# Kernel tuning notes

Measured on AMD Instinct MI355X. Metric: run time of the kernel, lower is better.

Reference implementation:

```python
import jax, jax.numpy as jnp
import numpy as np

N_NODES = 16384
N_EDGES = 65536
B = 256
L = 1000
BN_EPS = 1e-5


def _bn_last(h, g, b, m, v):
    # BatchNorm1d in eval mode over last (feature) axis
    return (h - m) / jnp.sqrt(v + BN_EPS) * g + b


def _bn_chan(h, g, b, m, v):
    # BatchNorm1d in eval mode over channel axis of [N, C, W]
    inv = g / jnp.sqrt(v + BN_EPS)
    return (h - m[None, :, None]) * inv[None, :, None] + b[None, :, None]


def _conv1d(x, W, b):
    # x: [N, C, W], W: [O, I, K], stride 1, VALID
    y = jax.lax.conv_general_dilated(x, W, (1,), 'VALID',
                                     dimension_numbers=('NCH', 'OIH', 'NCH'))
    return y + b[None, :, None]


def _forward(x, g1_W1, g1_b1, g1_W2, g1_b2, gW1, gb1, gW2, gb2,
             bn_gamma, bn_beta, bn_mean, bn_var, fcxd_W, fcxd_b, embed,
             c1_W, c1_b, c2_W, c2_b, c3_W, c3_b,
             cbn_gamma, cbn_beta, cbn_mean, cbn_var, fcxc_W, fcxc_b,
             bnfc_gamma, bnfc_beta, bnfc_mean, bnfc_var,
             fc1_W, fc1_b, fc2_W, fc2_b, out_W, out_b,
             edge_index, batch, target):
    src, dst = edge_index[0], edge_index[1]
    # GIN layer 1: out_i = MLP(x_i + sum_{j->i} x_j)  (eps = 0)
    agg = jax.ops.segment_sum(x[src], dst, num_segments=N_NODES)
    h = x + agg
    h = jnp.maximum(h @ g1_W1 + g1_b1, 0.0) @ g1_W2 + g1_b2
    h = _bn_last(jnp.maximum(h, 0.0), bn_gamma[0], bn_beta[0], bn_mean[0], bn_var[0])
    # GIN layers 2..5 (stacked params)
    for i in range(4):
        agg = jax.ops.segment_sum(h[src], dst, num_segments=N_NODES)
        t = h + agg
        t = jnp.maximum(t @ gW1[i] + gb1[i], 0.0) @ gW2[i] + gb2[i]
        h = _bn_last(jnp.maximum(t, 0.0), bn_gamma[i + 1], bn_beta[i + 1],
                     bn_mean[i + 1], bn_var[i + 1])
    # global_add_pool over graph ids
    pooled = jax.ops.segment_sum(h, batch, num_segments=B)          # [B, 32]
    xd = jnp.maximum(pooled @ fcxd_W + fcxd_b, 0.0)                 # [B, 128] (dropout: eval)
    # protein branch
    emb = embed[target]                                             # [B, L, 128]
    xd2 = jnp.broadcast_to(xd[:, None, :], (B, L, xd.shape[-1]))
    xc = jnp.concatenate([emb, xd2], axis=-1).transpose(0, 2, 1)    # [B, 256, L]
    conv_params = [(c1_W, c1_b), (c2_W, c2_b), (c3_W, c3_b)]
    for i in range(3):
        xc = _conv1d(xc, conv_params[i][0], conv_params[i][1])
        xc = jnp.maximum(_bn_chan(xc, cbn_gamma[i], cbn_beta[i],
                                  cbn_mean[i], cbn_var[i]), 0.0)
    xcm = jnp.max(xc, axis=-1)                                      # global max pool -> [B, 32]
    xcf = jnp.maximum(_bn_last(xcm @ fcxc_W + fcxc_b,
                               bnfc_gamma, bnfc_beta, bnfc_mean, bnfc_var), 0.0)
    z = jnp.concatenate([xd, xcf], axis=1)                          # [B, 256]
    z = jnp.maximum(z @ fc1_W + fc1_b, 0.0)
    z = jnp.maximum(z @ fc2_W + fc2_b, 0.0)
    return z @ out_W + out_b                                        # [B, 1]


def setup_inputs() -> dict:
    key = jax.random.key(0)
    ks = list(jax.random.split(key, 48))
    it = iter(range(48))
    f32 = jnp.float32

    def rn(sh, s=0.1):
        return jax.random.normal(ks[next(it)], sh, dtype=f32) * s

    def un(sh):
        return jax.random.uniform(ks[next(it)], sh, dtype=f32, minval=0.5, maxval=1.5)

    inp = {}
    inp['x'] = jax.random.normal(ks[next(it)], (N_NODES, 78), dtype=f32)
    inp['edge_index'] = jax.random.randint(ks[next(it)], (2, N_EDGES), 0, N_NODES, dtype=jnp.int32)
    inp['batch'] = jnp.sort(jax.random.randint(ks[next(it)], (N_NODES,), 0, B, dtype=jnp.int32))
    inp['target'] = jax.random.randint(ks[next(it)], (B, L), 0, 26, dtype=jnp.int32)
    inp['g1_W1'] = rn((78, 32)); inp['g1_b1'] = rn((32,))
    inp['g1_W2'] = rn((32, 32)); inp['g1_b2'] = rn((32,))
    inp['gW1'] = rn((4, 32, 32)); inp['gb1'] = rn((4, 32))
    inp['gW2'] = rn((4, 32, 32)); inp['gb2'] = rn((4, 32))
    inp['bn_gamma'] = un((5, 32)); inp['bn_beta'] = rn((5, 32))
    inp['bn_mean'] = rn((5, 32)); inp['bn_var'] = un((5, 32))
    inp['fcxd_W'] = rn((32, 128)); inp['fcxd_b'] = rn((128,))
    inp['embed'] = rn((26, 128), 1.0)
    inp['c1_W'] = rn((32, 256, 16)); inp['c1_b'] = rn((32,))
    inp['c2_W'] = rn((32, 32, 16)); inp['c2_b'] = rn((32,))
    inp['c3_W'] = rn((32, 32, 16)); inp['c3_b'] = rn((32,))
    inp['cbn_gamma'] = un((3, 32)); inp['cbn_beta'] = rn((3, 32))
    inp['cbn_mean'] = rn((3, 32)); inp['cbn_var'] = un((3, 32))
    inp['fcxc_W'] = rn((32, 128)); inp['fcxc_b'] = rn((128,))
    inp['bnfc_gamma'] = un((128,)); inp['bnfc_beta'] = rn((128,))
    inp['bnfc_mean'] = rn((128,)); inp['bnfc_var'] = un((128,))
    inp['fc1_W'] = rn((256, 1024)); inp['fc1_b'] = rn((1024,))
    inp['fc2_W'] = rn((1024, 256)); inp['fc2_b'] = rn((256,))
    inp['out_W'] = rn((256, 1)); inp['out_b'] = rn((1,))
    return inp


def reference(x, edge_index, batch, target, g1_W1, g1_b1, g1_W2, g1_b2,
              gW1, gb1, gW2, gb2, bn_gamma, bn_beta, bn_mean, bn_var,
              fcxd_W, fcxd_b, embed, c1_W, c1_b, c2_W, c2_b, c3_W, c3_b,
              cbn_gamma, cbn_beta, cbn_mean, cbn_var, fcxc_W, fcxc_b,
              bnfc_gamma, bnfc_beta, bnfc_mean, bnfc_var,
              fc1_W, fc1_b, fc2_W, fc2_b, out_W, out_b):
    return _forward(x, g1_W1, g1_b1, g1_W2, g1_b2, gW1, gb1, gW2, gb2,
                    bn_gamma, bn_beta, bn_mean, bn_var, fcxd_W, fcxd_b, embed,
                    c1_W, c1_b, c2_W, c2_b, c3_W, c3_b,
                    cbn_gamma, cbn_beta, cbn_mean, cbn_var, fcxc_W, fcxc_b,
                    bnfc_gamma, bnfc_beta, bnfc_mean, bnfc_var,
                    fc1_W, fc1_b, fc2_W, fc2_b, out_W, out_b,
                    edge_index, batch, target)
```

## Files before the change

### kernel.cpp

```cpp
#include <hip/hip_runtime.h>
#include <hip/hip_bf16.h>

typedef __hip_bfloat16 bf16;
__device__ __forceinline__ float b2f(bf16 v){ return __bfloat162float(v); }

typedef __attribute__((ext_vector_type(8))) short s8v;
typedef __attribute__((ext_vector_type(4))) float f4v;

#define N_NODES 16384
#define N_EDGES 65536
#define NB 256
#define LSEQ 1000
#define BN_EPS 1e-5f
#define W1O 985
#define W2O 970
#define W3O 955

__device__ int g_isf32;

__device__ __forceinline__ float LD(const void* p, int i, int f){
    return f ? ((const float*)p)[i] : b2f(((const bf16*)p)[i]);
}

__device__ __forceinline__ unsigned short f2b(float x){
    unsigned u = __float_as_uint(x);
    return (unsigned short)((u + 0x7FFFu + ((u >> 16) & 1u)) >> 16);
}
__device__ __forceinline__ float bb2f(unsigned short h){
    return __uint_as_float(((unsigned)h) << 16);
}

__device__ float g_hA[N_NODES*32];
__device__ float g_hB[N_NODES*32];
__device__ float g_xd[NB*128];
__device__ float g_P[16*26*32];
__device__ float g_wsum[32*128];
__device__ float g_xdb[NB*32];
__device__ float g_xcm[NB*32];
__device__ __attribute__((aligned(16))) unsigned short g_wf[2][32768];
__device__ int g_deg[N_NODES];
__device__ int g_cur[N_NODES];
__device__ int g_rowptr[N_NODES + 1];
__device__ int g_csrc[N_EDGES];
__device__ int g_gstart[NB + 1];

#define PREP_BLOCKS 2305

__global__ __launch_bounds__(256) void k_prep(
    const void* x, const int* __restrict__ ei, const int* __restrict__ batch,
    const void* g1W1)
{
    __shared__ float sW1[78*32];
    __shared__ float sx[8][78];
    __shared__ int s_cnt;
    int tid = threadIdx.x, bid = blockIdx.x;

    if (tid == 0) s_cnt = 0;
    __syncthreads();
    {
        const unsigned short* u = (const unsigned short*)x;
        int bad = 0;
        for (int i = tid; i < 512; i += 256){
            unsigned short h = u[i];
            int ex = (h >> 7) & 0xFF;
            if (!(h == 0 || (ex >= 96 && ex <= 142))) bad++;
        }
        if (bad) atomicAdd(&s_cnt, bad);
    }
    __syncthreads();
    const int F = (s_cnt > 50) ? 1 : 0;
    if (bid == 0 && tid == 0) g_isf32 = F;

    if (bid < 1){
        int b = tid;
        int lo = 0, hi = N_NODES;
        while (lo < hi){ int mid = (lo + hi) >> 1; if (batch[mid] < b) lo = mid + 1; else hi = mid; }
        g_gstart[b] = lo;
        if (b == 0) g_gstart[NB] = N_NODES;
    } else if (bid < 257){
        int e = (bid - 1)*256 + tid;
        atomicAdd(&g_deg[ei[N_EDGES + e]], 1);
    } else {
        for (int i = tid; i < 78*32; i += 256) sW1[i] = LD(g1W1, i, F);
        int nodeBase = (bid - 257)*8;
        for (int i = tid; i < 8*78; i += 256){
            int ln = i / 78, f = i - ln*78;
            sx[ln][f] = LD(x, (nodeBase + ln)*78 + f, F);
        }
        __syncthreads();
        int ln = tid >> 5, j = tid & 31;
        float a = 0.f;
        #pragma unroll 6
        for (int i = 0; i < 78; i++) a += sx[ln][i] * sW1[i*32 + j];
        g_hA[(nodeBase + ln)*32 + j] = a;
    }
}

__global__ __launch_bounds__(1024) void k_scan(){
    __shared__ int part[1024];
    int t = threadIdx.x;
    int base = t*16;
    int s = 0;
    #pragma unroll
    for (int i = 0; i < 16; i++) s += g_deg[base + i];
    part[t] = s;
    __syncthreads();
    for (int off = 1; off < 1024; off <<= 1){
        int v = (t >= off) ? part[t - off] : 0;
        __syncthreads();
        part[t] += v;
        __syncthreads();
    }
    int run = (t == 0) ? 0 : part[t - 1];
    for (int i = 0; i < 16; i++){
        g_rowptr[base + i] = run;
        g_cur[base + i] = run;
        run += g_deg[base + i];
        g_deg[base + i] = 0;
    }
    if (t == 1023) g_rowptr[N_NODES] = run;
}
__global__ void k_fill(const int* __restrict__ ei){
    int e = blockIdx.x*256 + threadIdx.x;
    int d = ei[N_EDGES + e];
    int slot = atomicAdd(&g_cur[d], 1);
    g_csrc[slot] = ei[e];
}

__device__ __forceinline__ float csr_gather(const float* hin, int n, int j){
    int rs = g_rowptr[n];
    int deg = g_rowptr[n + 1] - rs;
    float agg = 0.f;
    for (int base = 0; base < deg; base += 32){
        int cnt = deg - base; if (cnt > 32) cnt = 32;
        int myidx = (j < cnt) ? g_csrc[rs + base + j] : 0;
        for (int e = 0; e < cnt; e++){
            int src = __shfl(myidx, e, 32);
            agg += hin[src*32 + j];
        }
    }
    return agg;
}

#define GIN1B_GIN 2048
#define GIN1B_EXTRA 356

__global__ __launch_bounds__(256) void k_gin1b(
    const void* b1, const void* W2, const void* b2,
    const void* bng, const void* bnb, const void* bnm, const void* bnv,
    const void* embed, const void* c1W, const void* c2W, const void* c3W)
{
    const int F = g_isf32;
    int tid = threadIdx.x, bid = blockIdx.x;

    if (bid >= GIN1B_GIN){
        int t = bid - GIN1B_GIN;
        if (t < 256){
            int idx = t*256 + tid;
            int sel = idx >> 15;
            int r = idx & 32767;
            int j = r & 7;
            int lane = (r >> 3) & 63;
            int hl = (r >> 9) & 1;
            int ogrp = (r >> 10) & 1;
            int ktg = r >> 11;
            int c = (lane >> 4)*8 + j;
            int o = ogrp*16 + (lane & 15);
            const void* Wt = sel ? c3W : c2W;
            float wv = LD(Wt, o*512 + c*16 + ktg, F);
            unsigned short h = f2b(wv);
            g_wf[sel][r] = hl ? f2b(wv - bb2f(h)) : h;
        } else if (t < 308){
            int idx = (t - 256)*256 + tid;
            int k = idx & 15, o = (idx >> 4) & 31, tt = idx >> 9;
            float acc = 0.f;
            for (int c = 0; c < 128; c++)
                acc += LD(embed, tt*128 + c, F) * LD(c1W, o*4096 + c*16 + k, F);
            g_P[(k*26 + tt)*32 + o] = acc;
        } else if (t < 324){
            int idx = (t - 308)*256 + tid;
            int o = idx >> 7, c = idx & 127;
            float a = 0.f;
            #pragma unroll
            for (int k = 0; k < 16; k++) a += LD(c1W, o*4096 + (128 + c)*16 + k, F);
            g_wsum[o*128 + c] = a;
        } else {
            int i = (t - 324)*256 + tid;
            g_xcm[i] = 0.f;
        }
        return;
    }

    __shared__ float sW2[32*32];
    __shared__ float sb1[32], sb2[32], sA[32], sB[32];
    __shared__ float st[8][32];
    for (int i = tid; i < 1024; i += 256) sW2[i] = LD(W2, i, F);
    if (tid < 32){
        sb1[tid] = LD(b1, tid, F); sb2[tid] = LD(b2, tid, F);
        float inv = LD(bng, tid, F) * rsqrtf(LD(bnv, tid, F) + BN_EPS);
        sA[tid] = inv;
        sB[tid] = LD(bnb, tid, F) - LD(bnm, tid, F) * inv;
    }
    __syncthreads();
    int ln = tid >> 5, j = tid & 31;
    int n = bid*8 + ln;
    float agg = csr_gather(g_hA, n, j);
    st[ln][j] = fmaxf(g_hA[n*32 + j] + agg + sb1[j], 0.f);
    __syncthreads();
    float t2 = sb2[j];
    #pragma unroll
    for (int i = 0; i < 32; i++) t2 += st[ln][i] * sW2[i*32 + j];
    t2 = fmaxf(t2, 0.f);
    g_hB[n*32 + j] = t2 * sA[j] + sB[j];
}

__global__ __launch_bounds__(256) void k_gin32L(
    const void* W1, const void* b1, const void* W2, const void* b2,
    const void* bng, const void* bnb, const void* bnm, const void* bnv, int l)
{
    const int F = g_isf32;
    const float* hin = (l & 1) ? g_hA : g_hB;
    float* hout = (l & 1) ? g_hB : g_hA;
    const int oW = l*1024, ob = l*32, obn = (l+1)*32;
    __shared__ float sW1[32*32], sW2[32*32];
    __shared__ float sb1[32], sb2[32], sA[32], sB[32];
    __shared__ float sh[8][32], st[8][32];
    int tid = threadIdx.x;
    for (int i = tid; i < 1024; i += 256){ sW1[i] = LD(W1, oW + i, F); sW2[i] = LD(W2, oW + i, F); }
    if (tid < 32){
        sb1[tid] = LD(b1, ob + tid, F); sb2[tid] = LD(b2, ob + tid, F);
        float inv = LD(bng, obn + tid, F) * rsqrtf(LD(bnv, obn + tid, F) + BN_EPS);
        sA[tid] = inv;
        sB[tid] = LD(bnb, obn + tid, F) - LD(bnm, obn + tid, F) * inv;
    }
    int ln = tid >> 5, j = tid & 31;
    int n = blockIdx.x*8 + ln;
    float agg = csr_gather(hin, n, j);
    sh[ln][j] = hin[n*32 + j] + agg;
    __syncthreads();
    float t1 = sb1[j];
    #pragma unroll
    for (int i = 0; i < 32; i++) t1 += sh[ln][i] * sW1[i*32 + j];
    st[ln][j] = fmaxf(t1, 0.f);
    __syncthreads();
    float t2 = sb2[j];
    #pragma unroll
    for (int i = 0; i < 32; i++) t2 += st[ln][i] * sW2[i*32 + j];
    t2 = fmaxf(t2, 0.f);
    hout[n*32 + j] = t2 * sA[j] + sB[j];
}

__global__ __launch_bounds__(256) void k_poolxd(const void* W, const void* bias,
                                                const void* c1b){
    const int F = g_isf32;
    __shared__ float red[8][32];
    __shared__ float sxd[128];
    int b = blockIdx.x, tid = threadIdx.x;
    int j = tid & 31, sub = tid >> 5;
    int s = g_gstart[b], e = g_gstart[b + 1];
    float a = 0.f;
    for (int n = s + sub; n < e; n += 8) a += g_hB[n*32 + j];
    red[sub][j] = a;
    __syncthreads();
    if (sub == 0){
        red[0][j] = red[0][j] + red[1][j] + red[2][j] + red[3][j]
                  + red[4][j] + red[5][j] + red[6][j] + red[7][j];
    }
    __syncthreads();
    if (tid < 128){
        float acc = LD(bias, tid, F);
        #pragma unroll
        for (int i = 0; i < 32; i++) acc += red[0][i] * LD(W, i*128 + tid, F);
        float xdv = fmaxf(acc, 0.f);
        g_xd[b*128 + tid] = xdv;
        sxd[tid] = xdv;
    }
    __syncthreads();
    if (tid < 32){
        float a2 = LD(c1b, tid, F);
        for (int c = 0; c < 128; c++) a2 += sxd[c] * g_wsum[tid*128 + c];
        g_xdb[b*32 + tid] = a2;
    }
}


#define FT_W 128
#define C1R 160
#define C2R 144
#define CPAD 40
#define STGN 176

__global__ __launch_bounds__(512, 6) void k_cfuse(
    const int* __restrict__ target,
    const void* g, const void* be, const void* m, const void* v,
    const void* c2b, const void* c3b)
{
    const int F = g_isf32;
    __shared__ int stg[STGN];
    __shared__ __attribute__((aligned(16))) unsigned short sC1h[C1R*CPAD];
    __shared__ __attribute__((aligned(16))) unsigned short sC1l[C1R*CPAD];
    __shared__ __attribute__((aligned(16))) unsigned short sC2h[C2R*CPAD];
    __shared__ __attribute__((aligned(16))) unsigned short sC2l[C2R*CPAD];
    __shared__ float sxb[32], sA1[32], sB1[32], sSc2[32], sOf2[32], sSc3[32], sOf3[32];
    int b = blockIdx.x >> 3;
    int tile = blockIdx.x & 7;
    int wbase = tile * FT_W;
    int tid = threadIdx.x;

    for (int i = tid; i < STGN; i += 512){
        int gi = wbase + i;
        stg[i] = (gi < LSEQ) ? target[b*LSEQ + gi] : 0;
    }
    if (tid < 32){
        sxb[tid] = g_xdb[b*32 + tid];
        float i1 = LD(g, tid, F) * rsqrtf(LD(v, tid, F) + BN_EPS);
        sA1[tid] = i1;
        sB1[tid] = LD(be, tid, F) - LD(m, tid, F) * i1;
        float i2 = LD(g, 32 + tid, F) * rsqrtf(LD(v, 32 + tid, F) + BN_EPS);
        sSc2[tid] = i2;
        sOf2[tid] = LD(be, 32 + tid, F) + (LD(c2b, tid, F) - LD(m, 32 + tid, F)) * i2;
        float i3 = LD(g, 64 + tid, F) * rsqrtf(LD(v, 64 + tid, F) + BN_EPS);
        sSc3[tid] = i3;
        sOf3[tid] = LD(be, 64 + tid, F) + (LD(c3b, tid, F) - LD(m, 64 + tid, F)) * i3;
    }
    __syncthreads();

    {
        int o = tid & 31, rsub = tid >> 5;
        float iA = sA1[o], iB = sB1[o], xb = sxb[o];
        for (int r0 = rsub; r0 < C1R; r0 += 32){
            int r1 = r0 + 16;
            float a0 = xb, a1 = xb;
            #pragma unroll
            for (int k = 0; k < 16; k++){
                a0 += g_P[(k*26 + stg[r0 + k])*32 + o];
                a1 += g_P[(k*26 + stg[r1 + k])*32 + o];
            }
            float v0 = (wbase + r0 < W1O) ? fmaxf(a0 * iA + iB, 0.f) : 0.f;
            float v1 = (wbase + r1 < W1O) ? fmaxf(a1 * iA + iB, 0.f) : 0.f;
            unsigned short h0 = f2b(v0), h1 = f2b(v1);
            sC1h[r0*CPAD + o] = h0;
            sC1l[r0*CPAD + o] = f2b(v0 - bb2f(h0));
            sC1h[r1*CPAD + o] = h1;
            sC1l[r1*CPAD + o] = f2b(v1 - bb2f(h1));
        }
    }
    __syncthreads();

    int lane = tid & 63;
    int wv = tid >> 6;
    int ml = lane & 15, quad = lane >> 4;
    int ogrp = wv & 1;
    int part = wv >> 1;
    int oo = ogrp*16 + ml;

    {
        const s8v* wfb = (const s8v*)&g_wf[0][0] + ogrp*128 + lane;
        int nmt = (part == 0) ? 3 : 2;
        f4v acc[3];
        #pragma unroll
        for (int i = 0; i < 3; i++) acc[i] = (f4v){0.f,0.f,0.f,0.f};
        s8v bhA = wfb[0],   blA = wfb[64];
        s8v bhB = wfb[256], blB = wfb[320];
        for (int ktg = 0; ktg < 16; ktg += 2){
            s8v ch = bhA, cl = blA;
            if (ktg + 2 < 16){ bhA = wfb[(ktg+2)*256]; blA = wfb[(ktg+2)*256 + 64]; }
            #pragma unroll
            for (int i = 0; i < 3; i++){
                if (i < nmt){
                    int row = (part + 4*i)*16 + ml + ktg;
                    int aidx = row*CPAD + quad*8;
                    s8v ah = *(const s8v*)&sC1h[aidx];
                    s8v al = *(const s8v*)&sC1l[aidx];
                    acc[i] = __builtin_amdgcn_mfma_f32_16x16x32_bf16(ah, ch, acc[i], 0, 0, 0);
                    acc[i] = __builtin_amdgcn_mfma_f32_16x16x32_bf16(ah, cl, acc[i], 0, 0, 0);
                    acc[i] = __builtin_amdgcn_mfma_f32_16x16x32_bf16(al, ch, acc[i], 0, 0, 0);
                }
            }
            s8v dh = bhB, dl = blB;
            if (ktg + 3 < 16){ bhB = wfb[(ktg+3)*256]; blB = wfb[(ktg+3)*256 + 64]; }
            #pragma unroll
            for (int i = 0; i < 3; i++){
                if (i < nmt){
                    int row = (part + 4*i)*16 + ml + ktg + 1;
                    int aidx = row*CPAD + quad*8;
                    s8v ah = *(const s8v*)&sC1h[aidx];
                    s8v al = *(const s8v*)&sC1l[aidx];
                    acc[i] = __builtin_amdgcn_mfma_f32_16x16x32_bf16(ah, dh, acc[i], 0, 0, 0);
                    acc[i] = __builtin_amdgcn_mfma_f32_16x16x32_bf16(ah, dl, acc[i], 0, 0, 0);
                    acc[i] = __builtin_amdgcn_mfma_f32_16x16x32_bf16(al, dh, acc[i], 0, 0, 0);
                }
            }
        }
        float sc = sSc2[oo], of = sOf2[oo];
        #pragma unroll
        for (int i = 0; i < 3; i++){
            if (i < nmt){
                int mt = part + 4*i;
                f4v a = acc[i];
                float ys[4] = {a.x, a.y, a.z, a.w};
                #pragma unroll
                for (int rr = 0; rr < 4; rr++){
                    int row = mt*16 + quad*4 + rr;
                    float y = fmaxf(ys[rr]*sc + of, 0.f);
                    unsigned short h = f2b(y);
                    sC2h[row*CPAD + oo] = h;
                    sC2l[row*CPAD + oo] = f2b(y - bb2f(h));
                }
            }
        }
    }
    __syncthreads();

    {
        const s8v* wfb = (const s8v*)&g_wf[1][0] + ogrp*128 + lane;
        f4v acc[2];
        #pragma unroll
        for (int i = 0; i < 2; i++) acc[i] = (f4v){0.f,0.f,0.f,0.f};
        s8v bhA = wfb[0],   blA = wfb[64];
        s8v bhB = wfb[256], blB = wfb[320];
        for (int ktg = 0; ktg < 16; ktg += 2){
            s8v ch = bhA, cl = blA;
            if (ktg + 2 < 16){ bhA = wfb[(ktg+2)*256]; blA = wfb[(ktg+2)*256 + 64]; }
            #pragma unroll
            for (int i = 0; i < 2; i++){
                int row = (part + 4*i)*16 + ml + ktg;
                int aidx = row*CPAD + quad*8;
                s8v ah = *(const s8v*)&sC2h[aidx];
                s8v al = *(const s8v*)&sC2l[aidx];
                acc[i] = __builtin_amdgcn_mfma_f32_16x16x32_bf16(ah, ch, acc[i], 0, 0, 0);
                acc[i] = __builtin_amdgcn_mfma_f32_16x16x32_bf16(ah, cl, acc[i], 0, 0, 0);
                acc[i] = __builtin_amdgcn_mfma_f32_16x16x32_bf16(al, ch, acc[i], 0, 0, 0);
            }
            s8v dh = bhB, dl = blB;
            if (ktg + 3 < 16){ bhB = wfb[(ktg+3)*256]; blB = wfb[(ktg+3)*256 + 64]; }
            #pragma unroll
            for (int i = 0; i < 2; i++){
                int row = (part + 4*i)*16 + ml + ktg + 1;
                int aidx = row*CPAD + quad*8;
                s8v ah = *(const s8v*)&sC2h[aidx];
                s8v al = *(const s8v*)&sC2l[aidx];
                acc[i] = __builtin_amdgcn_mfma_f32_16x16x32_bf16(ah, dh, acc[i], 0, 0, 0);
                acc[i] = __builtin_amdgcn_mfma_f32_16x16x32_bf16(ah, dl, acc[i], 0, 0, 0);
                acc[i] = __builtin_amdgcn_mfma_f32_16x16x32_bf16(al, dh, acc[i], 0, 0, 0);
            }
        }
        float sc = sSc3[oo], of = sOf3[oo];
        #pragma unroll
        for (int i = 0; i < 2; i++){
            int mt = part + 4*i;
            int w0 = wbase + mt*16 + quad*4;
            f4v a = acc[i];
            float y0 = fmaxf(a.x*sc + of, 0.f);
            float y1 = fmaxf(a.y*sc + of, 0.f);
            float y2 = fmaxf(a.z*sc + of, 0.f);
            float y3 = fmaxf(a.w*sc + of, 0.f);
            if (w0 < W3O){
                float mx = y0;
                if (w0+1 < W3O) mx = fmaxf(mx, y1);
                if (w0+2 < W3O) mx = fmaxf(mx, y2);
                if (w0+3 < W3O) mx = fmaxf(mx, y3);
                atomicMax((int*)&g_xcm[b*32 + oo], __float_as_int(mx));
            }
        }
    }
}


__global__ __launch_bounds__(1024) void k_tail(
    const void* fcxcW, const void* fcxcb,
    const void* bg, const void* bb, const void* bm, const void* bv,
    const void* fc1W, const void* fc1b,
    const void* fc2W, const void* fc2b,
    const void* outW, const void* outb, void* out)
{
    const int F = g_isf32;
    __shared__ float sz[256];
    __shared__ float z1s[1024];
    __shared__ float sp[4][256];
    int b = blockIdx.x, t = threadIdx.x;
    if (t < 128) sz[t] = g_xd[b*128 + t];
    else if (t < 256){
        int j = t - 128;
        float a = LD(fcxcb, j, F);
        #pragma unroll
        for (int i = 0; i < 32; i++) a += g_xcm[b*32 + i] * LD(fcxcW, i*128 + j, F);
        float inv = LD(bg, j, F) * rsqrtf(LD(bv, j, F) + BN_EPS);
        a = (a - LD(bm, j, F)) * inv + LD(bb, j, F);
        sz[t] = fmaxf(a, 0.f);
    }
    __syncthreads();
    float a = LD(fc1b, t, F);
    for (int i = 0; i < 256; i++) a += sz[i] * LD(fc1W, i*1024 + t, F);
    z1s[t] = fmaxf(a, 0.f);
    __syncthreads();
    int j = t & 255, kq = t >> 8;
    float a2 = 0.f;
    #pragma unroll 8
    for (int i = 0; i < 256; i++)
        a2 += z1s[kq*256 + i] * LD(fc2W, (kq*256 + i)*256 + j, F);
    sp[kq][j] = a2;
    __syncthreads();
    if (t < 256){
        float z2 = fmaxf(sp[0][t] + sp[1][t] + sp[2][t] + sp[3][t] + LD(fc2b, t, F), 0.f);
        sp[0][t] = z2 * LD(outW, t, F);
    }
    __syncthreads();
    for (int s = 128; s > 0; s >>= 1){
        if (t < s) sp[0][t] += sp[0][t + s];
        __syncthreads();
    }
    if (t == 0){
        float r = sp[0][0] + LD(outb, 0, F);
        if (F) ((float*)out)[b] = r;
        else   ((bf16*)out)[b] = __float2bfloat16(r);
    }
}


extern "C" void kernel_launch(void* const* d_in, const int* in_sizes, int n_in,
                              void* d_out, int out_size, void* d_ws, size_t ws_size,
                              hipStream_t stream)
{
    (void)in_sizes; (void)n_in; (void)out_size; (void)d_ws; (void)ws_size;
    const void* x      = d_in[0];
    const int*  ei     = (const int*)d_in[1];
    const int*  batch  = (const int*)d_in[2];
    const int*  target = (const int*)d_in[3];
    const void* g1W1 = d_in[4];  const void* g1b1 = d_in[5];
    const void* g1W2 = d_in[6];  const void* g1b2 = d_in[7];
    const void* gW1  = d_in[8];  const void* gb1  = d_in[9];
    const void* gW2  = d_in[10]; const void* gb2  = d_in[11];
    const void* bng  = d_in[12]; const void* bnb  = d_in[13];
    const void* bnm  = d_in[14]; const void* bnv  = d_in[15];
    const void* fcxdW = d_in[16]; const void* fcxdb = d_in[17];
    const void* embed = d_in[18];
    const void* c1W = d_in[19]; const void* c1b = d_in[20];
    const void* c2W = d_in[21]; const void* c2b = d_in[22];
    const void* c3W = d_in[23]; const void* c3b = d_in[24];
    const void* cbng = d_in[25]; const void* cbnb = d_in[26];
    const void* cbnm = d_in[27]; const void* cbnv = d_in[28];
    const void* fcxcW = d_in[29]; const void* fcxcb = d_in[30];
    const void* bnfcg = d_in[31]; const void* bnfcb = d_in[32];
    const void* bnfcm = d_in[33]; const void* bnfcv = d_in[34];
    const void* fc1W = d_in[35]; const void* fc1b = d_in[36];
    const void* fc2W = d_in[37]; const void* fc2b = d_in[38];
    const void* outW = d_in[39]; const void* outb = d_in[40];

    k_prep<<<PREP_BLOCKS, 256, 0, stream>>>(x, ei, batch, g1W1);
    k_scan<<<1, 1024, 0, stream>>>();
    k_fill<<<N_EDGES/256, 256, 0, stream>>>(ei);
    k_gin1b<<<GIN1B_GIN + GIN1B_EXTRA, 256, 0, stream>>>(
        g1b1, g1W2, g1b2, bng, bnb, bnm, bnv, embed, c1W, c2W, c3W);
    for (int l = 0; l < 4; l++){
        k_gin32L<<<N_NODES/8, 256, 0, stream>>>(gW1, gb1, gW2, gb2,
                                                bng, bnb, bnm, bnv, l);
    }
    k_poolxd<<<NB, 256, 0, stream>>>(fcxdW, fcxdb, c1b);
    k_cfuse<<<NB*8, 512, 0, stream>>>(target, cbng, cbnb, cbnm, cbnv, c2b, c3b);
    k_tail<<<NB, 1024, 0, stream>>>(fcxcW, fcxcb, bnfcg, bnfcb, bnfcm, bnfcv,
                                    fc1W, fc1b, fc2W, fc2b, outW, outb, d_out);
}
```

Baseline: 400.5 us.

## Remap conv MFMA waves to cover both output groups, batch two samples per tail block

In the fused conv kernel, each wave now computes both 16-channel output groups for its own 16-row tile. Each A fragment loaded from LDS is therefore reused across two weight fragments, which replaces the old split where waves covered 2-3 interleaved row tiles of a single output group. The aim is fewer LDS reads per MFMA and less loop-control overhead, at the cost of uneven work, since wave 0 handles an extra tile. The tail MLP kernel now processes two batch samples per block so each fc1/fc2 weight load is shared, halving weight traffic but also halving the number of blocks.

Measured after the change: 427.0 us. 1.07x slower.

```diff
diff --git a/kernel.cpp b/kernel.cpp
--- a/kernel.cpp
+++ b/kernel.cpp
@@ -290,6 +290,8 @@
 #define CPAD 40
 #define STGN 176
 
+#define MFMA_BF16 __builtin_amdgcn_mfma_f32_16x16x32_bf16
+
 __global__ __launch_bounds__(512, 6) void k_cfuse(
     const int* __restrict__ target,
     const void* g, const void* be, const void* m, const void* v,
@@ -350,118 +352,128 @@
     int lane = tid & 63;
     int wv = tid >> 6;
     int ml = lane & 15, quad = lane >> 4;
-    int ogrp = wv & 1;
-    int part = wv >> 1;
-    int oo = ogrp*16 + ml;
 
     {
-        const s8v* wfb = (const s8v*)&g_wf[0][0] + ogrp*128 + lane;
-        int nmt = (part == 0) ? 3 : 2;
-        f4v acc[3];
-        #pragma unroll
-        for (int i = 0; i < 3; i++) acc[i] = (f4v){0.f,0.f,0.f,0.f};
-        s8v bhA = wfb[0],   blA = wfb[64];
-        s8v bhB = wfb[256], blB = wfb[320];
-        for (int ktg = 0; ktg < 16; ktg += 2){
-            s8v ch = bhA, cl = blA;
-            if (ktg + 2 < 16){ bhA = wfb[(ktg+2)*256]; blA = wfb[(ktg+2)*256 + 64]; }
+        const s8v* wf0 = (const s8v*)&g_wf[0][0] + lane;
+        const s8v* wf1 = (const s8v*)&g_wf[0][0] + 128 + lane;
+        int has2 = (wv == 0);
+        f4v a00 = (f4v){0.f,0.f,0.f,0.f}, a01 = (f4v){0.f,0.f,0.f,0.f};
+        f4v a10 = (f4v){0.f,0.f,0.f,0.f}, a11 = (f4v){0.f,0.f,0.f,0.f};
+        s8v nh0 = wf0[0], nl0 = wf0[64];
+        s8v nh1 = wf1[0], nl1 = wf1[64];
+        for (int ktg = 0; ktg < 16; ktg++){
+            s8v bh0 = nh0, bl0 = nl0, bh1 = nh1, bl1 = nl1;
+            if (ktg < 15){
+                nh0 = wf0[(ktg+1)*256]; nl0 = wf0[(ktg+1)*256 + 64];
+                nh1 = wf1[(ktg+1)*256]; nl1 = wf1[(ktg+1)*256 + 64];
+            }
+            {
+                int row = wv*16 + ml + ktg;
+                int aidx = row*CPAD + quad*8;
+                s8v ah = *(const s8v*)&sC1h[aidx];
+                s8v al = *(const s8v*)&sC1l[aidx];
+                a00 = MFMA_BF16(ah, bh0, a00, 0, 0, 0);
+                a00 = MFMA_BF16(ah, bl0, a00, 0, 0, 0);
+                a00 = MFMA_BF16(al, bh0, a00, 0, 0, 0);
+                a01 = MFMA_BF16(ah, bh1, a01, 0, 0, 0);
+                a01 = MFMA_BF16(ah, bl1, a01, 0, 0, 0);
+                a01 = MFMA_BF16(al, bh1, a01, 0, 0, 0);
+            }
+            if (has2){
+                int row = 128 + ml + ktg;
+                int aidx = row*CPAD + quad*8;
+                s8v ah = *(const s8v*)&sC1h[aidx];
+                s8v al = *(const s8v*)&sC1l[aidx];
+                a10 = MFMA_BF16(ah, bh0, a10, 0, 0, 0);
+                a10 = MFMA_BF16(ah, bl0, a10, 0, 0, 0);
+                a10 = MFMA_BF16(al, bh0, a10, 0, 0, 0);
+                a11 = MFMA_BF16(ah, bh1, a11, 0, 0, 0);
+                a11 = MFMA_BF16(ah, bl1, a11, 0, 0, 0);
+                a11 = MFMA_BF16(al, bh1, a11, 0, 0, 0);
+            }
+        }
+        float sc0 = sSc2[ml],      of0 = sOf2[ml];
+        float sc1 = sSc2[16 + ml], of1 = sOf2[16 + ml];
+        {
+            float y00[4] = {a00.x, a00.y, a00.z, a00.w};
+            float y01[4] = {a01.x, a01.y, a01.z, a01.w};
             #pragma unroll
-            for (int i = 0; i < 3; i++){
-                if (i < nmt){
-                    int row = (part + 4*i)*16 + ml + ktg;
-                    int aidx = row*CPAD + quad*8;
-                    s8v ah = *(const s8v*)&sC1h[aidx];
-                    s8v al = *(const s8v*)&sC1l[aidx];
-                    acc[i] = __builtin_amdgcn_mfma_f32_16x16x32_bf16(ah, ch, acc[i], 0, 0, 0);
-                    acc[i] = __builtin_amdgcn_mfma_f32_16x16x32_bf16(ah, cl, acc[i], 0, 0, 0);
-                    acc[i] = __builtin_amdgcn_mfma_f32_16x16x32_bf16(al, ch, acc[i], 0, 0, 0);
-                }
+            for (int rr = 0; rr < 4; rr++){
+                int row = wv*16 + quad*4 + rr;
+                float u0 = fmaxf(y00[rr]*sc0 + of0, 0.f);
+                unsigned short h0 = f2b(u0);
+                sC2h[row*CPAD + ml] = h0;
+                sC2l[row*CPAD + ml] = f2b(u0 - bb2f(h0));
+                float u1 = fmaxf(y01[rr]*sc1 + of1, 0.f);
+                unsigned short h1 = f2b(u1);
+                sC2h[row*CPAD + 16 + ml] = h1;
+                sC2l[row*CPAD + 16 + ml] = f2b(u1 - bb2f(h1));
             }
-            s8v dh = bhB, dl = blB;
-            if (ktg + 3 < 16){ bhB = wfb[(ktg+3)*256]; blB = wfb[(ktg+3)*256 + 64]; }
+        }
+        if (has2){
+            float y10[4] = {a10.x, a10.y, a10.z, a10.w};
+            float y11[4] = {a11.x, a11.y, a11.z, a11.w};
             #pragma unroll
-            for (int i = 0; i < 3; i++){
-                if (i < nmt){
-                    int row = (part + 4*i)*16 + ml + ktg + 1;
-                    int aidx = row*CPAD + quad*8;
-                    s8v ah = *(const s8v*)&sC1h[aidx];
-                    s8v al = *(const s8v*)&sC1l[aidx];
-                    acc[i] = __builtin_amdgcn_mfma_f32_16x16x32_bf16(ah, dh, acc[i], 0, 0, 0);
-                    acc[i] = __builtin_amdgcn_mfma_f32_16x16x32_bf16(ah, dl, acc[i], 0, 0, 0);
-                    acc[i] = __builtin_amdgcn_mfma_f32_16x16x32_bf16(al, dh, acc[i], 0, 0, 0);
-                }
+            for (int rr = 0; rr < 4; rr++){
+                int row = 128 + quad*4 + rr;
+                float u0 = fmaxf(y10[rr]*sc0 + of0, 0.f);
+                unsigned short h0 = f2b(u0);
+                sC2h[row*CPAD + ml] = h0;
+                sC2l[row*CPAD + ml] = f2b(u0 - bb2f(h0));
+                float u1 = fmaxf(y11[rr]*sc1 + of1, 0.f);
+                unsigned short h1 = f2b(u1);
+                sC2h[row*CPAD + 16 + ml] = h1;
+                sC2l[row*CPAD + 16 + ml] = f2b(u1 - bb2f(h1));
             }
         }
-        float sc = sSc2[oo], of = sOf2[oo];
-        #pragma unroll
-        for (int i = 0; i < 3; i++){
-            if (i < nmt){
-                int mt = part + 4*i;
-                f4v a = acc[i];
-                float ys[4] = {a.x, a.y, a.z, a.w};
-                #pragma unroll
-                for (int rr = 0; rr < 4; rr++){
-                    int row = mt*16 + quad*4 + rr;
-                    float y = fmaxf(ys[rr]*sc + of, 0.f);
-                    unsigned short h = f2b(y);
-                    sC2h[row*CPAD + oo] = h;
-                    sC2l[row*CPAD + oo] = f2b(y - bb2f(h));
-                }
+    }
+    __syncthreads();
+
+    {
+        const s8v* wf0 = (const s8v*)&g_wf[1][0] + lane;
+        const s8v* wf1 = (const s8v*)&g_wf[1][0] + 128 + lane;
+        f4v c0 = (f4v){0.f,0.f,0.f,0.f}, c1 = (f4v){0.f,0.f,0.f,0.f};
+        s8v nh0 = wf0[0], nl0 = wf0[64];
+        s8v nh1 = wf1[0], nl1 = wf1[64];
+        for (int ktg = 0; ktg < 16; ktg++){
+            s8v bh0 = nh0, bl0 = nl0, bh1 = nh1, bl1 = nl1;
+            if (ktg < 15){
+                nh0 = wf0[(ktg+1)*256]; nl0 = wf0[(ktg+1)*256 + 64];
+                nh1 = wf1[(ktg+1)*256]; nl1 = wf1[(ktg+1)*256 + 64];
             }
-        }
-    }
-    __syncthreads();
-
-    {
-        const s8v* wfb = (const s8v*)&g_wf[1][0] + ogrp*128 + lane;
-        f4v acc[2];
-        #pragma unroll
-        for (int i = 0; i < 2; i++) acc[i] = (f4v){0.f,0.f,0.f,0.f};
-        s8v bhA = wfb[0],   blA = wfb[64];
-        s8v bhB = wfb[256], blB = wfb[320];
-        for (int ktg = 0; ktg < 16; ktg += 2){
-            s8v ch = bhA, cl = blA;
-            if (ktg + 2 < 16){ bhA = wfb[(ktg+2)*256]; blA = wfb[(ktg+2)*256 + 64]; }
-            #pragma unroll
-            for (int i = 0; i < 2; i++){
-                int row = (part + 4*i)*16 + ml + ktg;
-                int aidx = row*CPAD + quad*8;
-                s8v ah = *(const s8v*)&sC2h[aidx];
-                s8v al = *(const s8v*)&sC2l[aidx];
-                acc[i] = __builtin_amdgcn_mfma_f32_16x16x32_bf16(ah, ch, acc[i], 0, 0, 0);
-                acc[i] = __builtin_amdgcn_mfma_f32_16x16x32_bf16(ah, cl, acc[i], 0, 0, 0);
-                acc[i] = __builtin_amdgcn_mfma_f32_16x16x32_bf16(al, ch, acc[i], 0, 0, 0);
-            }
-            s8v dh = bhB, dl = blB;
-            if (ktg + 3 < 16){ bhB = wfb[(ktg+3)*256]; blB = wfb[(ktg+3)*256 + 64]; }
-            #pragma unroll
-            for (int i = 0; i < 2; i++){
-                int row = (part + 4*i)*16 + ml + ktg + 1;
-                int aidx = row*CPAD + quad*8;
-                s8v ah = *(const s8v*)&sC2h[aidx];
-                s8v al = *(const s8v*)&sC2l[aidx];
-                acc[i] = __builtin_amdgcn_mfma_f32_16x16x32_bf16(ah, dh, acc[i], 0, 0, 0);
-                acc[i] = __builtin_amdgcn_mfma_f32_16x16x32_bf16(ah, dl, acc[i], 0, 0, 0);
-                acc[i] = __builtin_amdgcn_mfma_f32_16x16x32_bf16(al, dh, acc[i], 0, 0, 0);
-            }
-        }
-        float sc = sSc3[oo], of = sOf3[oo];
-        #pragma unroll
-        for (int i = 0; i < 2; i++){
-            int mt = part + 4*i;
-            int w0 = wbase + mt*16 + quad*4;
-            f4v a = acc[i];
-            float y0 = fmaxf(a.x*sc + of, 0.f);
-            float y1 = fmaxf(a.y*sc + of, 0.f);
-            float y2 = fmaxf(a.z*sc + of, 0.f);
-            float y3 = fmaxf(a.w*sc + of, 0.f);
-            if (w0 < W3O){
-                float mx = y0;
-                if (w0+1 < W3O) mx = fmaxf(mx, y1);
-                if (w0+2 < W3O) mx = fmaxf(mx, y2);
-                if (w0+3 < W3O) mx = fmaxf(mx, y3);
-                atomicMax((int*)&g_xcm[b*32 + oo], __float_as_int(mx));
-            }
+            int row = wv*16 + ml + ktg;
+            int aidx = row*CPAD + quad*8;
+            s8v ah = *(const s8v*)&sC2h[aidx];
+            s8v al = *(const s8v*)&sC2l[aidx];
+            c0 = MFMA_BF16(ah, bh0, c0, 0, 0, 0);
+            c0 = MFMA_BF16(ah, bl0, c0, 0, 0, 0);
+            c0 = MFMA_BF16(al, bh0, c0, 0, 0, 0);
+            c1 = MFMA_BF16(ah, bh1, c1, 0, 0, 0);
+            c1 = MFMA_BF16(ah, bl1, c1, 0, 0, 0);
+            c1 = MFMA_BF16(al, bh1, c1, 0, 0, 0);
+        }
+        float sc0 = sSc3[ml],      of0 = sOf3[ml];
+        float sc1 = sSc3[16 + ml], of1 = sOf3[16 + ml];
+        int w0 = wbase + wv*16 + quad*4;
+        if (w0 < W3O){
+            float p0 = fmaxf(c0.x*sc0 + of0, 0.f);
+            float p1 = fmaxf(c0.y*sc0 + of0, 0.f);
+            float p2 = fmaxf(c0.z*sc0 + of0, 0.f);
+            float p3 = fmaxf(c0.w*sc0 + of0, 0.f);
+            float mx = p0;
+            if (w0+1 < W3O) mx = fmaxf(mx, p1);
+            if (w0+2 < W3O) mx = fmaxf(mx, p2);
+            if (w0+3 < W3O) mx = fmaxf(mx, p3);
+            atomicMax((int*)&g_xcm[b*32 + ml], __float_as_int(mx));
+            float q0 = fmaxf(c1.x*sc1 + of1, 0.f);
+            float q1 = fmaxf(c1.y*sc1 + of1, 0.f);
+            float q2 = fmaxf(c1.z*sc1 + of1, 0.f);
+            float q3 = fmaxf(c1.w*sc1 + of1, 0.f);
+            float my = q0;
+            if (w0+1 < W3O) my = fmaxf(my, q1);
+            if (w0+2 < W3O) my = fmaxf(my, q2);
+            if (w0+3 < W3O) my = fmaxf(my, q3);
+            atomicMax((int*)&g_xcm[b*32 + 16 + ml], __float_as_int(my));
         }
     }
 }
@@ -475,45 +487,74 @@
     const void* outW, const void* outb, void* out)
 {
     const int F = g_isf32;
-    __shared__ float sz[256];
-    __shared__ float z1s[1024];
-    __shared__ float sp[4][256];
-    int b = blockIdx.x, t = threadIdx.x;
-    if (t < 128) sz[t] = g_xd[b*128 + t];
-    else if (t < 256){
+    __shared__ float sz0[256], sz1[256];
+    __shared__ float z1s0[1024], z1s1[1024];
+    __shared__ float sp0[4][256], sp1[4][256];
+    int b0 = blockIdx.x*2, b1 = b0 + 1, t = threadIdx.x;
+    if (t < 128){
+        sz0[t] = g_xd[b0*128 + t];
+        sz1[t] = g_xd[b1*128 + t];
+    } else if (t < 256){
         int j = t - 128;
-        float a = LD(fcxcb, j, F);
+        float a0 = LD(fcxcb, j, F), a1 = a0;
         #pragma unroll
-        for (int i = 0; i < 32; i++) a += g_xcm[b*32 + i] * LD(fcxcW, i*128 + j, F);
+        for (int i = 0; i < 32; i++){
+            float w = LD(fcxcW, i*128 + j, F);
+            a0 += g_xcm[b0*32 + i] * w;
+            a1 += g_xcm[b1*32 + i] * w;
+        }
         float inv = LD(bg, j, F) * rsqrtf(LD(bv, j, F) + BN_EPS);
-        a = (a - LD(bm, j, F)) * inv + LD(bb, j, F);
-        sz[t] = fmaxf(a, 0.f);
-    }
-    __syncthreads();
-    float a = LD(fc1b, t, F);
-    for (int i = 0; i < 256; i++) a += sz[i] * LD(fc1W, i*1024 + t, F);
-    z1s[t] = fmaxf(a, 0.f);
+        float bm_ = LD(bm, j, F), bb_ = LD(bb, j, F);
+        sz0[t] = fmaxf((a0 - bm_) * inv + bb_, 0.f);
+        sz1[t] = fmaxf((a1 - bm_) * inv + bb_, 0.f);
+    }
+    __syncthreads();
+    {
+        float a0 = LD(fc1b, t, F), a1 = a0;
+        for (int i = 0; i < 256; i++){
+            float w = LD(fc1W, i*1024 + t, F);
+            a0 += sz0[i] * w;
+            a1 += sz1[i] * w;
+        }
+        z1s0[t] = fmaxf(a0, 0.f);
+        z1s1[t] = fmaxf(a1, 0.f);
+    }
     __syncthreads();
     int j = t & 255, kq = t >> 8;
-    float a2 = 0.f;
-    #pragma unroll 8
-    for (int i = 0; i < 256; i++)
-        a2 += z1s[kq*256 + i] * LD(fc2W, (kq*256 + i)*256 + j, F);
-    sp[kq][j] = a2;
+    {
+        float a20 = 0.f, a21 = 0.f;
+        #pragma unroll 8
+        for (int i = 0; i < 256; i++){
+            float w = LD(fc2W, (kq*256 + i)*256 + j, F);
+            a20 += z1s0[kq*256 + i] * w;
+            a21 += z1s1[kq*256 + i] * w;
+        }
+        sp0[kq][j] = a20;
+        sp1[kq][j] = a21;
+    }
     __syncthreads();
     if (t < 256){
-        float z2 = fmaxf(sp[0][t] + sp[1][t] + sp[2][t] + sp[3][t] + LD(fc2b, t, F), 0.f);
-        sp[0][t] = z2 * LD(outW, t, F);
+        float bias = LD(fc2b, t, F), ow = LD(outW, t, F);
+        float z20 = fmaxf(sp0[0][t] + sp0[1][t] + sp0[2][t] + sp0[3][t] + bias, 0.f);
+        float z21 = fmaxf(sp1[0][t] + sp1[1][t] + sp1[2][t] + sp1[3][t] + bias, 0.f);
+        sp0[0][t] = z20 * ow;
+        sp1[0][t] = z21 * ow;
     }
     __syncthreads();
     for (int s = 128; s > 0; s >>= 1){
-        if (t < s) sp[0][t] += sp[0][t + s];
+        if (t < s){
+            sp0[0][t] += sp0[0][t + s];
+            sp1[0][t] += sp1[0][t + s];
+        }
         __syncthreads();
     }
     if (t == 0){
-        float r = sp[0][0] + LD(outb, 0, F);
-        if (F) ((float*)out)[b] = r;
-        else   ((bf16*)out)[b] = __float2bfloat16(r);
+        float ob = LD(outb, 0, F);
+        float r0 = sp0[0][0] + ob;
+        float r1 = sp1[0][0] + ob;
+        if (F){ ((float*)out)[b0] = r0; ((float*)out)[b1] = r1; }
+        else  { ((bf16*)out)[b0] = __float2bfloat16(r0);
+                ((bf16*)out)[b1] = __float2bfloat16(r1); }
     }
 }
 
@@ -558,6 +599,6 @@
     }
     k_poolxd<<<NB, 256, 0, stream>>>(fcxdW, fcxdb, c1b);
     k_cfuse<<<NB*8, 512, 0, stream>>>(target, cbng, cbnb, cbnm, cbnv, c2b, c3b);
-    k_tail<<<NB, 1024, 0, stream>>>(fcxcW, fcxcb, bnfcg, bnfcb, bnfcm, bnfcv,
-                                    fc1W, fc1b, fc2W, fc2b, outW, outb, d_out);
-}
+    k_tail<<<NB/2, 1024, 0, stream>>>(fcxcW, fcxcb, bnfcg, bnfcb, bnfcm, bnfcv,
+                                      fc1W, fc1b, fc2W, fc2b, outW, outb, d_out);
+}
```

## Fuse pooling into conv and tail kernels; process two graphs per tail block

Applied to the files above, without the earlier changes.

Removes the separate pooling/xd kernel. Each conv tile block now recomputes the graph pooling, the xd projection and the conv1 bias contribution itself, and the tail kernel recomputes pooling and xd too. The tail kernel now handles two graphs per block so each fc1/fc2 weight load is shared by two samples. This saves one launch and halves weight traffic in the tail, at the cost of redundant pooling work (8x in the conv kernel) and more shared memory.

After: 414.4 us. 3.5% more time.

```diff
diff --git a/kernel.cpp b/kernel.cpp
--- a/kernel.cpp
+++ b/kernel.cpp
@@ -32,10 +32,8 @@
 
 __device__ float g_hA[N_NODES*32];
 __device__ float g_hB[N_NODES*32];
-__device__ float g_xd[NB*128];
 __device__ float g_P[16*26*32];
 __device__ float g_wsum[32*128];
-__device__ float g_xdb[NB*32];
 __device__ float g_xcm[NB*32];
 __device__ __attribute__((aligned(16))) unsigned short g_wf[2][32768];
 __device__ int g_deg[N_NODES];
@@ -250,39 +248,6 @@
     hout[n*32 + j] = t2 * sA[j] + sB[j];
 }
 
-__global__ __launch_bounds__(256) void k_poolxd(const void* W, const void* bias,
-                                                const void* c1b){
-    const int F = g_isf32;
-    __shared__ float red[8][32];
-    __shared__ float sxd[128];
-    int b = blockIdx.x, tid = threadIdx.x;
-    int j = tid & 31, sub = tid >> 5;
-    int s = g_gstart[b], e = g_gstart[b + 1];
-    float a = 0.f;
-    for (int n = s + sub; n < e; n += 8) a += g_hB[n*32 + j];
-    red[sub][j] = a;
-    __syncthreads();
-    if (sub == 0){
-        red[0][j] = red[0][j] + red[1][j] + red[2][j] + red[3][j]
-                  + red[4][j] + red[5][j] + red[6][j] + red[7][j];
-    }
-    __syncthreads();
-    if (tid < 128){
-        float acc = LD(bias, tid, F);
-        #pragma unroll
-        for (int i = 0; i < 32; i++) acc += red[0][i] * LD(W, i*128 + tid, F);
-        float xdv = fmaxf(acc, 0.f);
-        g_xd[b*128 + tid] = xdv;
-        sxd[tid] = xdv;
-    }
-    __syncthreads();
-    if (tid < 32){
-        float a2 = LD(c1b, tid, F);
-        for (int c = 0; c < 128; c++) a2 += sxd[c] * g_wsum[tid*128 + c];
-        g_xdb[b*32 + tid] = a2;
-    }
-}
-
 
 #define FT_W 128
 #define C1R 160
@@ -293,7 +258,8 @@
 __global__ __launch_bounds__(512, 6) void k_cfuse(
     const int* __restrict__ target,
     const void* g, const void* be, const void* m, const void* v,
-    const void* c2b, const void* c3b)
+    const void* c2b, const void* c3b,
+    const void* fcxdW, const void* fcxdb, const void* c1b)
 {
     const int F = g_isf32;
     __shared__ int stg[STGN];
@@ -302,6 +268,8 @@
     __shared__ __attribute__((aligned(16))) unsigned short sC2h[C2R*CPAD];
     __shared__ __attribute__((aligned(16))) unsigned short sC2l[C2R*CPAD];
     __shared__ float sxb[32], sA1[32], sB1[32], sSc2[32], sOf2[32], sSc3[32], sOf3[32];
+    __shared__ float pred[8][32];
+    __shared__ float pxd[128];
     int b = blockIdx.x >> 3;
     int tile = blockIdx.x & 7;
     int wbase = tile * FT_W;
@@ -312,7 +280,6 @@
         stg[i] = (gi < LSEQ) ? target[b*LSEQ + gi] : 0;
     }
     if (tid < 32){
-        sxb[tid] = g_xdb[b*32 + tid];
         float i1 = LD(g, tid, F) * rsqrtf(LD(v, tid, F) + BN_EPS);
         sA1[tid] = i1;
         sB1[tid] = LD(be, tid, F) - LD(m, tid, F) * i1;
@@ -322,6 +289,34 @@
         float i3 = LD(g, 64 + tid, F) * rsqrtf(LD(v, 64 + tid, F) + BN_EPS);
         sSc3[tid] = i3;
         sOf3[tid] = LD(be, 64 + tid, F) + (LD(c3b, tid, F) - LD(m, 64 + tid, F)) * i3;
+    }
+    {
+        int s = g_gstart[b], e = g_gstart[b + 1];
+        if (tid < 256){
+            int j = tid & 31, sub = tid >> 5;
+            float a = 0.f;
+            for (int n = s + sub; n < e; n += 8) a += g_hB[n*32 + j];
+            pred[sub][j] = a;
+        }
+        __syncthreads();
+        if (tid < 32){
+            int j = tid;
+            pred[0][j] = pred[0][j] + pred[1][j] + pred[2][j] + pred[3][j]
+                       + pred[4][j] + pred[5][j] + pred[6][j] + pred[7][j];
+        }
+        __syncthreads();
+        if (tid < 128){
+            float acc = LD(fcxdb, tid, F);
+            #pragma unroll
+            for (int i = 0; i < 32; i++) acc += pred[0][i] * LD(fcxdW, i*128 + tid, F);
+            pxd[tid] = fmaxf(acc, 0.f);
+        }
+        __syncthreads();
+        if (tid < 32){
+            float a2 = LD(c1b, tid, F);
+            for (int c = 0; c < 128; c++) a2 += pxd[c] * g_wsum[tid*128 + c];
+            sxb[tid] = a2;
+        }
     }
     __syncthreads();
 
@@ -472,48 +467,107 @@
     const void* bg, const void* bb, const void* bm, const void* bv,
     const void* fc1W, const void* fc1b,
     const void* fc2W, const void* fc2b,
-    const void* outW, const void* outb, void* out)
+    const void* outW, const void* outb, void* out,
+    const void* fcxdW, const void* fcxdb)
 {
     const int F = g_isf32;
-    __shared__ float sz[256];
-    __shared__ float z1s[1024];
-    __shared__ float sp[4][256];
-    int b = blockIdx.x, t = threadIdx.x;
-    if (t < 128) sz[t] = g_xd[b*128 + t];
-    else if (t < 256){
+    __shared__ float red0[8][32], red1[8][32];
+    __shared__ float sz0[256], sz1[256];
+    __shared__ float z1s0[1024], z1s1[1024];
+    __shared__ float sp0[4][256], sp1[4][256];
+    int b0 = blockIdx.x*2, b1 = b0 + 1, t = threadIdx.x;
+
+    if (t < 512){
+        int j = t & 31, sub = (t >> 5) & 7;
+        int bg_ = (t < 256) ? b0 : b1;
+        int s = g_gstart[bg_], e = g_gstart[bg_ + 1];
+        float a = 0.f;
+        for (int n = s + sub; n < e; n += 8) a += g_hB[n*32 + j];
+        if (t < 256) red0[sub][j] = a; else red1[sub][j] = a;
+    }
+    __syncthreads();
+    if (t < 32){
+        int j = t;
+        red0[0][j] = red0[0][j] + red0[1][j] + red0[2][j] + red0[3][j]
+                   + red0[4][j] + red0[5][j] + red0[6][j] + red0[7][j];
+    } else if (t < 64){
+        int j = t - 32;
+        red1[0][j] = red1[0][j] + red1[1][j] + red1[2][j] + red1[3][j]
+                   + red1[4][j] + red1[5][j] + red1[6][j] + red1[7][j];
+    }
+    __syncthreads();
+    if (t < 128){
+        float acc = LD(fcxdb, t, F);
+        #pragma unroll
+        for (int i = 0; i < 32; i++) acc += red0[0][i] * LD(fcxdW, i*128 + t, F);
+        sz0[t] = fmaxf(acc, 0.f);
+    } else if (t < 256){
         int j = t - 128;
-        float a = LD(fcxcb, j, F);
+        float acc = LD(fcxdb, j, F);
         #pragma unroll
-        for (int i = 0; i < 32; i++) a += g_xcm[b*32 + i] * LD(fcxcW, i*128 + j, F);
+        for (int i = 0; i < 32; i++) acc += red1[0][i] * LD(fcxdW, i*128 + j, F);
+        sz1[j] = fmaxf(acc, 0.f);
+    } else if (t < 384){
+        int j = t - 256;
+        float a0 = LD(fcxcb, j, F), a1 = a0;
+        #pragma unroll
+        for (int i = 0; i < 32; i++){
+            float w = LD(fcxcW, i*128 + j, F);
+            a0 += g_xcm[b0*32 + i] * w;
+            a1 += g_xcm[b1*32 + i] * w;
+        }
         float inv = LD(bg, j, F) * rsqrtf(LD(bv, j, F) + BN_EPS);
-        a = (a - LD(bm, j, F)) * inv + LD(bb, j, F);
-        sz[t] = fmaxf(a, 0.f);
-    }
-    __syncthreads();
-    float a = LD(fc1b, t, F);
-    for (int i = 0; i < 256; i++) a += sz[i] * LD(fc1W, i*1024 + t, F);
-    z1s[t] = fmaxf(a, 0.f);
+        float bm_ = LD(bm, j, F), bb_ = LD(bb, j, F);
+        sz0[128 + j] = fmaxf((a0 - bm_) * inv + bb_, 0.f);
+        sz1[128 + j] = fmaxf((a1 - bm_) * inv + bb_, 0.f);
+    }
+    __syncthreads();
+    {
+        float a0 = LD(fc1b, t, F), a1 = a0;
+        for (int i = 0; i < 256; i++){
+            float w = LD(fc1W, i*1024 + t, F);
+            a0 += sz0[i] * w;
+            a1 += sz1[i] * w;
+        }
+        z1s0[t] = fmaxf(a0, 0.f);
+        z1s1[t] = fmaxf(a1, 0.f);
+    }
     __syncthreads();
     int j = t & 255, kq = t >> 8;
-    float a2 = 0.f;
-    #pragma unroll 8
-    for (int i = 0; i < 256; i++)
-        a2 += z1s[kq*256 + i] * LD(fc2W, (kq*256 + i)*256 + j, F);
-    sp[kq][j] = a2;
+    {
+        float a20 = 0.f, a21 = 0.f;
+        #pragma unroll 8
+        for (int i = 0; i < 256; i++){
+            float w = LD(fc2W, (kq*256 + i)*256 + j, F);
+            a20 += z1s0[kq*256 + i] * w;
+            a21 += z1s1[kq*256 + i] * w;
+        }
+        sp0[kq][j] = a20;
+        sp1[kq][j] = a21;
+    }
     __syncthreads();
     if (t < 256){
-        float z2 = fmaxf(sp[0][t] + sp[1][t] + sp[2][t] + sp[3][t] + LD(fc2b, t, F), 0.f);
-        sp[0][t] = z2 * LD(outW, t, F);
+        float bias = LD(fc2b, t, F), ow = LD(outW, t, F);
+        float z20 = fmaxf(sp0[0][t] + sp0[1][t] + sp0[2][t] + sp0[3][t] + bias, 0.f);
+        float z21 = fmaxf(sp1[0][t] + sp1[1][t] + sp1[2][t] + sp1[3][t] + bias, 0.f);
+        sp0[0][t] = z20 * ow;
+        sp1[0][t] = z21 * ow;
     }
     __syncthreads();
     for (int s = 128; s > 0; s >>= 1){
-        if (t < s) sp[0][t] += sp[0][t + s];
+        if (t < s){
+            sp0[0][t] += sp0[0][t + s];
+            sp1[0][t] += sp1[0][t + s];
+        }
         __syncthreads();
     }
     if (t == 0){
-        float r = sp[0][0] + LD(outb, 0, F);
-        if (F) ((float*)out)[b] = r;
-        else   ((bf16*)out)[b] = __float2bfloat16(r);
+        float ob = LD(outb, 0, F);
+        float r0 = sp0[0][0] + ob;
+        float r1 = sp1[0][0] + ob;
+        if (F){ ((float*)out)[b0] = r0; ((float*)out)[b1] = r1; }
+        else  { ((bf16*)out)[b0] = __float2bfloat16(r0);
+                ((bf16*)out)[b1] = __float2bfloat16(r1); }
     }
 }
 
@@ -556,8 +610,9 @@
         k_gin32L<<<N_NODES/8, 256, 0, stream>>>(gW1, gb1, gW2, gb2,
                                                 bng, bnb, bnm, bnv, l);
     }
-    k_poolxd<<<NB, 256, 0, stream>>>(fcxdW, fcxdb, c1b);
-    k_cfuse<<<NB*8, 512, 0, stream>>>(target, cbng, cbnb, cbnm, cbnv, c2b, c3b);
-    k_tail<<<NB, 1024, 0, stream>>>(fcxcW, fcxcb, bnfcg, bnfcb, bnfcm, bnfcv,
-                                    fc1W, fc1b, fc2W, fc2b, outW, outb, d_out);
-}
+    k_cfuse<<<NB*8, 512, 0, stream>>>(target, cbng, cbnb, cbnm, cbnv, c2b, c3b,
+                                      fcxdW, fcxdb, c1b);
+    k_tail<<<NB/2, 1024, 0, stream>>>(fcxcW, fcxcb, bnfcg, bnfcb, bnfcm, bnfcv,
+                                      fc1W, fc1b, fc2W, fc2b, outW, outb, d_out,
+                                      fcxdW, fcxdb);
+}
```
